# Kernel optimization log

Measured on AMD Instinct MI355X. Metric: run time of the kernel, lower is better.

## Reference

```python
import jax, jax.numpy as jnp
import numpy as np

N = 4_194_304  # total points
C = 2          # classes: 0=ground, 1=plant
B = 8          # number of point clouds in the batch
SIGMA_L = 0.1
SIGMA_R = 0.4
CLAMP_FACTOR = 2.0
MIN_VAL = 0.1
FOCAL_GAMMA = 2.0
FOCAL_ALPHA = 1.0
LOSS_WEIGHT = 1.0


def setup_inputs() -> dict:
    key = jax.random.key(0)
    k1, k2, k3 = jax.random.split(key, 3)
    pred = jax.random.normal(k1, (N, C), dtype=jnp.float32)
    coord = jax.random.normal(k2, (N, 3), dtype=jnp.float32)
    segment = jax.random.randint(k3, (N,), 0, C, dtype=jnp.int32)
    # pointcept-style cumulative offsets: equal-sized clouds, offset[-1] == N
    offset = (jnp.arange(1, B + 1, dtype=jnp.int32) * (N // B))
    return {"pred": pred, "coord": coord, "segment": segment, "offset": offset}


def _gauss_weights(z, segment, batch):
    # per-cloud z_ground_max (fallback: z.min) and z_plant_min (fallback: z.max)
    neg_inf = jnp.array(-jnp.inf, z.dtype)
    pos_inf = jnp.array(jnp.inf, z.dtype)
    gmax = jax.ops.segment_max(jnp.where(segment == 0, z, neg_inf), batch, num_segments=B)
    pmin = jax.ops.segment_min(jnp.where(segment == 1, z, pos_inf), batch, num_segments=B)
    has_g = jax.ops.segment_sum((segment == 0).astype(z.dtype), batch, num_segments=B) > 0
    has_p = jax.ops.segment_sum((segment == 1).astype(z.dtype), batch, num_segments=B) > 0
    zmin = jax.ops.segment_min(z, batch, num_segments=B)
    zmax = jax.ops.segment_max(z, batch, num_segments=B)
    g = jnp.where(has_g, gmax, zmin)
    p = jnp.where(has_p, pmin, zmax)
    mu_b = g + (p - g) * 0.5  # (B,)
    mu = mu_b[batch]          # (N,)
    d = z - mu
    w_left = jnp.exp(-(d * d) / (2.0 * SIGMA_L * SIGMA_L))
    w_right = jnp.exp(-(d * d) / (2.0 * SIGMA_R * SIGMA_R))
    w_right = jnp.where(d > CLAMP_FACTOR * SIGMA_R, jnp.array(MIN_VAL, z.dtype), w_right)
    return jnp.where(z <= mu, w_left, w_right)


def reference(pred, coord, segment, offset):
    n = pred.shape[0]
    # offset2batch: per-point batch id from cumulative offsets
    batch = jnp.searchsorted(offset, jnp.arange(n, dtype=offset.dtype), side='right')
    # cross entropy (reduction='none')
    logp = jax.nn.log_softmax(pred, axis=1)              # (N, C)
    logp_t = jnp.take_along_axis(logp, segment[:, None], axis=1)[:, 0]  # (N,)
    seg_loss = (-logp_t) * LOSS_WEIGHT
    # focal reweighting (computed under no_grad in the original)
    p_t = jax.lax.stop_gradient(jnp.exp(logp_t))
    focal_weight = FOCAL_ALPHA * (1.0 - p_t) ** FOCAL_GAMMA
    seg_loss = seg_loss * focal_weight
    # asymmetric gaussian z-weighting, segment-conditioned per cloud
    weights = _gauss_weights(coord[:, 2], segment, batch)
    return jnp.mean(seg_loss * weights)
```

## Files before the change

### kernel.cpp

```cpp
#include <hip/hip_runtime.h>
#include <math.h>

#define T   1024
#define NB  512

__device__ __forceinline__ unsigned enc_f(float f) {
    unsigned b = __float_as_uint(f);
    return (b & 0x80000000u) ? ~b : (b | 0x80000000u);
}
__device__ __forceinline__ float dec_f(unsigned u) {
    unsigned b = (u & 0x80000000u) ? (u ^ 0x80000000u) : ~u;
    return __uint_as_float(b);
}
#define ENC_NEG_INF 0x007FFFFFu
#define ENC_POS_INF 0xFF800000u
__device__ __forceinline__ unsigned ident_w(int w) {
    return (w < 8 || w >= 24) ? ENC_NEG_INF : ENC_POS_INF;
}

#define SLOT(base, blk) ((base) + 64 + (blk) * 32)
#define PART_W  20000u

#define CNT_B(ii, bdst) do { bdst = 0; \
    _Pragma("unroll") for (int j_ = 0; j_ < 8; ++j_) bdst += ((ii) >= roff[j_]); } while (0)

#define FLUSH_LDS(bb, g_, p_, mn_, mx_) do { \
    atomicMax(&s_stats[      (bb)], enc_f(g_));  \
    atomicMin(&s_stats[ 8  + (bb)], enc_f(p_));  \
    atomicMin(&s_stats[16  + (bb)], enc_f(mn_)); \
    atomicMax(&s_stats[24  + (bb)], enc_f(mx_)); } while (0)

#define STAT4(z0, z1, z2, z3, s) do { \
    lmn = fminf(lmn, fminf(fminf(z0, z1), fminf(z2, z3))); \
    lmx = fmaxf(lmx, fmaxf(fmaxf(z0, z1), fmaxf(z2, z3))); \
    lg = fmaxf(lg, ((s).x == 0) ? z0 : -INFINITY); \
    lg = fmaxf(lg, ((s).y == 0) ? z1 : -INFINITY); \
    lg = fmaxf(lg, ((s).z == 0) ? z2 : -INFINITY); \
    lg = fmaxf(lg, ((s).w == 0) ? z3 : -INFINITY); \
    lp = fminf(lp, ((s).x != 0) ? z0 : INFINITY); \
    lp = fminf(lp, ((s).y != 0) ? z1 : INFINITY); \
    lp = fminf(lp, ((s).z != 0) ? z2 : INFINITY); \
    lp = fminf(lp, ((s).w != 0) ? z3 : INFINITY); } while (0)

__device__ __forceinline__ float point_loss(float p0, float p1, int s, float z, float mu) {
    float margin = (s == 0) ? (p0 - p1) : (p1 - p0);
    float t   = __expf(-margin);
    float den = 1.0f + t;
    float inv = __builtin_amdgcn_rcpf(den);
    float om  = t * inv;
    float loss = __logf(den) * om * om;
    float d  = z - mu;
    float cf = (z <= mu) ? 50.0f : 3.125f;
    float w  = __expf(-d * d * cf);
    if (z > mu && d > 0.8f) w = 0.1f;
    return loss * w;
}

__global__ __launch_bounds__(T, 8) void k_stats(
        const float* __restrict__ coord, const int* __restrict__ segment,
        const int* __restrict__ offset, unsigned* __restrict__ ws, int n, int nb) {
    __shared__ unsigned s_stats[32];
    const int tid = threadIdx.x;
    if (tid < 32) s_stats[tid] = ident_w(tid);
    int roff[8];
    #pragma unroll
    for (int j = 0; j < 8; ++j) roff[j] = (j < nb) ? offset[j] : 0x7FFFFFFF;
    __syncthreads();

    int chunk = (n + (int)gridDim.x - 1) / (int)gridDim.x;
    chunk = (chunk + 3) & ~3;
    const int start = blockIdx.x * chunk;
    const int end   = min(n, start + chunk);

    if (start < end) {
        int ba = 0, bb = 0;
        #pragma unroll
        for (int j = 0; j < 8; ++j) { ba += (start >= roff[j]); bb += ((end - 1) >= roff[j]); }
        float lg = -INFINITY, lp = INFINITY, lmn = INFINITY, lmx = -INFINITY;

        if (ba == bb && (end - start) == 8 * T) {
            const float4* c4 = (const float4*)coord;
            const int4*   s4 = (const int4*)segment;
            const int q0 = (start >> 2) + tid, q1 = q0 + T;
            float4 a0 = c4[3 * q0 + 0], b0 = c4[3 * q0 + 1], c0 = c4[3 * q0 + 2];
            float4 a1 = c4[3 * q1 + 0], b1 = c4[3 * q1 + 1], c1 = c4[3 * q1 + 2];
            int4   s0 = s4[q0],        s1 = s4[q1];
            const float x0 = a0.z, x1 = b0.y, x2 = c0.x, x3 = c0.w;
            STAT4(x0, x1, x2, x3, s0);
            const float y0 = a1.z, y1 = b1.y, y2 = c1.x, y3 = c1.w;
            STAT4(y0, y1, y2, y3, s1);
            #pragma unroll
            for (int m = 32; m; m >>= 1) {
                lg  = fmaxf(lg,  __shfl_xor(lg,  m, 64));
                lp  = fminf(lp,  __shfl_xor(lp,  m, 64));
                lmn = fminf(lmn, __shfl_xor(lmn, m, 64));
                lmx = fmaxf(lmx, __shfl_xor(lmx, m, 64));
            }
            if ((tid & 63) == 0) FLUSH_LDS(ba, lg, lp, lmn, lmx);
        } else if (ba == bb && ((end - start) % (4 * T) == 0)) {
            const float4* c4 = (const float4*)coord;
            const int4*   s4 = (const int4*)segment;
            for (int p0 = start; p0 < end; p0 += 4 * T) {
                const int q = (p0 >> 2) + tid;
                float4 a = c4[3 * q + 0], b = c4[3 * q + 1], c = c4[3 * q + 2];
                int4   s = s4[q];
                const float x0 = a.z, x1 = b.y, x2 = c.x, x3 = c.w;
                STAT4(x0, x1, x2, x3, s);
            }
            #pragma unroll
            for (int m = 32; m; m >>= 1) {
                lg  = fmaxf(lg,  __shfl_xor(lg,  m, 64));
                lp  = fminf(lp,  __shfl_xor(lp,  m, 64));
                lmn = fminf(lmn, __shfl_xor(lmn, m, 64));
                lmx = fmaxf(lmx, __shfl_xor(lmx, m, 64));
            }
            if ((tid & 63) == 0) FLUSH_LDS(ba, lg, lp, lmn, lmx);
        } else {
            int curb = -1;
            for (int i = start + tid; i < end; i += T) {
                float z = coord[3 * i + 2]; int s = segment[i], b;
                CNT_B(i, b);
                if (b != curb) {
                    if (curb >= 0) FLUSH_LDS(curb, lg, lp, lmn, lmx);
                    lg = -INFINITY; lp = INFINITY; lmn = INFINITY; lmx = -INFINITY;
                    curb = b;
                }
                lmn = fminf(lmn, z); lmx = fmaxf(lmx, z);
                if (s == 0) lg = fmaxf(lg, z); else lp = fminf(lp, z);
            }
            if (curb >= 0) FLUSH_LDS(curb, lg, lp, lmn, lmx);
        }
    }
    __syncthreads();
    if (tid < 32) SLOT(ws, blockIdx.x)[tid] = s_stats[tid];
}

__global__ __launch_bounds__(T, 8) void k_loss(
        const float* __restrict__ pred, const float* __restrict__ coord,
        const int* __restrict__ segment, const int* __restrict__ offset,
        unsigned* __restrict__ ws, int n, int nb) {
    __shared__ unsigned s_comb[32];
    __shared__ float    s_mu[8];
    __shared__ float    s_part[T / 64];
    const int tid = threadIdx.x;
    int roff[8];
    #pragma unroll
    for (int j = 0; j < 8; ++j) roff[j] = (j < nb) ? offset[j] : 0x7FFFFFFF;

    if (tid < 32) s_comb[tid] = ident_w(tid);
    __syncthreads();
    {
        const int w = tid & 31, g = tid >> 5;
        unsigned v = ident_w(w);
        #pragma unroll
        for (int j = 0; j < NB / 32; ++j) {
            unsigned u = SLOT((const unsigned*)ws, g * (NB / 32) + j)[w];
            v = (w < 8 || w >= 24) ? max(v, u) : min(v, u);
        }
        if (w < 8 || w >= 24) atomicMax(&s_comb[w], v);
        else                  atomicMin(&s_comb[w], v);
    }
    __syncthreads();
    if (tid < 8) {
        unsigned ug = s_comb[tid], up = s_comb[8 + tid];
        float g = dec_f(ug), p = dec_f(up);
        if (ug == ENC_NEG_INF) g = dec_f(s_comb[16 + tid]);
        if (up == ENC_POS_INF) p = dec_f(s_comb[24 + tid]);
        s_mu[tid] = g + (p - g) * 0.5f;
    }
    __syncthreads();

    int chunk = (n + (int)gridDim.x - 1) / (int)gridDim.x;
    chunk = (chunk + 3) & ~3;
    const int start = blockIdx.x * chunk;
    const int end   = min(n, start + chunk);

    float lsum = 0.0f;
    if (start < end) {
        int ba = 0, bb = 0;
        #pragma unroll
        for (int j = 0; j < 8; ++j) { ba += (start >= roff[j]); bb += ((end - 1) >= roff[j]); }

        if (ba == bb && (end - start) == 8 * T) {
            const float mu = s_mu[ba];
            const float4* p4 = (const float4*)pred;
            const float4* c4 = (const float4*)coord;
            const int4*   s4 = (const int4*)segment;
            const int q0 = (start >> 2) + tid, q1 = q0 + T;
            float4 pa0 = p4[2 * q0 + 0], pb0 = p4[2 * q0 + 1];
            float4 pa1 = p4[2 * q1 + 0], pb1 = p4[2 * q1 + 1];
            float4 a0 = c4[3 * q0 + 0], b0 = c4[3 * q0 + 1], c0 = c4[3 * q0 + 2];
            float4 a1 = c4[3 * q1 + 0], b1 = c4[3 * q1 + 1], c1 = c4[3 * q1 + 2];
            int4   s0 = s4[q0],        s1 = s4[q1];
            lsum += point_loss(pa0.x, pa0.y, s0.x, a0.z, mu);
            lsum += point_loss(pa0.z, pa0.w, s0.y, b0.y, mu);
            lsum += point_loss(pb0.x, pb0.y, s0.z, c0.x, mu);
            lsum += point_loss(pb0.z, pb0.w, s0.w, c0.w, mu);
            lsum += point_loss(pa1.x, pa1.y, s1.x, a1.z, mu);
            lsum += point_loss(pa1.z, pa1.w, s1.y, b1.y, mu);
            lsum += point_loss(pb1.x, pb1.y, s1.z, c1.x, mu);
            lsum += point_loss(pb1.z, pb1.w, s1.w, c1.w, mu);
        } else if (ba == bb && ((end - start) % (4 * T) == 0)) {
            const float mu = s_mu[ba];
            const float4* p4 = (const float4*)pred;
            const float4* c4 = (const float4*)coord;
            const int4*   s4 = (const int4*)segment;
            for (int p0 = start; p0 < end; p0 += 4 * T) {
                const int q = (p0 >> 2) + tid;
                float4 pa = p4[2 * q + 0], pb = p4[2 * q + 1];
                float4 a  = c4[3 * q + 0], b = c4[3 * q + 1], c = c4[3 * q + 2];
                int4   s  = s4[q];
                lsum += point_loss(pa.x, pa.y, s.x, a.z, mu);
                lsum += point_loss(pa.z, pa.w, s.y, b.y, mu);
                lsum += point_loss(pb.x, pb.y, s.z, c.x, mu);
                lsum += point_loss(pb.z, pb.w, s.w, c.w, mu);
            }
        } else {
            const float2* pred2 = (const float2*)pred;
            for (int i = start + tid; i < end; i += T) {
                int b; CNT_B(i, b);
                float2 pp = pred2[i];
                lsum += point_loss(pp.x, pp.y, segment[i], coord[3 * i + 2], s_mu[b]);
            }
        }
    }

    #pragma unroll
    for (int off = 32; off > 0; off >>= 1) lsum += __shfl_down(lsum, off, 64);
    if ((tid & 63) == 0) s_part[tid >> 6] = lsum;
    __syncthreads();
    if (tid == 0) {
        float t = 0.0f;
        #pragma unroll
        for (int wv = 0; wv < T / 64; ++wv) t += s_part[wv];
        ((float*)(ws + PART_W))[blockIdx.x] = t;
    }
}

__global__ __launch_bounds__(NB) void k_final(
        const unsigned* __restrict__ ws, float* __restrict__ out, int n) {
    __shared__ float sp[NB];
    const int tid = threadIdx.x;
    sp[tid] = ((const float*)(ws + PART_W))[tid];
    __syncthreads();
    if (tid == 0) {
        double v = 0.0;
        for (int i = 0; i < NB; ++i) v += (double)sp[i];
        out[0] = (float)(v / (double)n);
    }
}

extern "C" void kernel_launch(void* const* d_in, const int* in_sizes, int n_in,
                              void* d_out, int out_size, void* d_ws, size_t ws_size,
                              hipStream_t stream) {
    const float* pred    = (const float*)d_in[0];
    const float* coord   = (const float*)d_in[1];
    const int*   segment = (const int*)d_in[2];
    const int*   offset  = (const int*)d_in[3];
    const int n  = in_sizes[2];
    const int nb = in_sizes[3];
    unsigned* ws = (unsigned*)d_ws;

    hipLaunchKernelGGL(k_stats, dim3(NB), dim3(T), 0, stream,
                       coord, segment, offset, ws, n, nb);
    hipLaunchKernelGGL(k_loss, dim3(NB), dim3(T), 0, stream,
                       pred, coord, segment, offset, ws, n, nb);
    hipLaunchKernelGGL(k_final, dim3(1), dim3(NB), 0, stream,
                       ws, (float*)d_out, n);
}
```

Before: 131.0 us.

## Use many small blocks and add hierarchical stats-combine kernel

Blocks shrink from 1024 to 256 threads, and the grid grows from 512 to 4096 blocks, each covering 4*T points. This is meant to spread work more evenly over the CUs and raise occupancy. A new k_mu kernel reduces the 4096 per-block stat records into 32 intermediate records, so each k_loss block reads only 32 records instead of every block's partials. The final reduction changes to sum 4096 partials. The cost is an extra kernel launch and a second reduction level.

```diff
diff --git a/kernel.cpp b/kernel.cpp
--- a/kernel.cpp
+++ b/kernel.cpp
@@ -1,8 +1,10 @@
 #include <hip/hip_runtime.h>
 #include <math.h>
 
-#define T   1024
-#define NB  512
+#define T    256
+#define NB   4096
+#define NM   32
+#define RPM  (NB / NM)
 
 __device__ __forceinline__ unsigned enc_f(float f) {
     unsigned b = __float_as_uint(f);
@@ -19,7 +21,8 @@
 }
 
 #define SLOT(base, blk) ((base) + 64 + (blk) * 32)
-#define PART_W  20000u
+#define SREC(base, m)   ((base) + 131200u + (m) * 32)
+#define PART_W  140000u
 
 #define CNT_B(ii, bdst) do { bdst = 0; \
     _Pragma("unroll") for (int j_ = 0; j_ < 8; ++j_) bdst += ((ii) >= roff[j_]); } while (0)
@@ -56,7 +59,7 @@
     return loss * w;
 }
 
-__global__ __launch_bounds__(T, 8) void k_stats(
+__global__ __launch_bounds__(T) void k_stats(
         const float* __restrict__ coord, const int* __restrict__ segment,
         const int* __restrict__ offset, unsigned* __restrict__ ws, int n, int nb) {
     __shared__ unsigned s_stats[32];
@@ -78,17 +81,13 @@
         for (int j = 0; j < 8; ++j) { ba += (start >= roff[j]); bb += ((end - 1) >= roff[j]); }
         float lg = -INFINITY, lp = INFINITY, lmn = INFINITY, lmx = -INFINITY;
 
-        if (ba == bb && (end - start) == 8 * T) {
-            const float4* c4 = (const float4*)coord;
-            const int4*   s4 = (const int4*)segment;
-            const int q0 = (start >> 2) + tid, q1 = q0 + T;
-            float4 a0 = c4[3 * q0 + 0], b0 = c4[3 * q0 + 1], c0 = c4[3 * q0 + 2];
-            float4 a1 = c4[3 * q1 + 0], b1 = c4[3 * q1 + 1], c1 = c4[3 * q1 + 2];
-            int4   s0 = s4[q0],        s1 = s4[q1];
-            const float x0 = a0.z, x1 = b0.y, x2 = c0.x, x3 = c0.w;
-            STAT4(x0, x1, x2, x3, s0);
-            const float y0 = a1.z, y1 = b1.y, y2 = c1.x, y3 = c1.w;
-            STAT4(y0, y1, y2, y3, s1);
+        if (ba == bb && (end - start) == 4 * T) {
+            const float4* c4 = (const float4*)coord;
+            const int4*   s4 = (const int4*)segment;
+            const int q = (start >> 2) + tid;
+            float4 a = c4[3 * q + 0], b = c4[3 * q + 1], c = c4[3 * q + 2];
+            int4   s = s4[q];
+            STAT4(a.z, b.y, c.x, c.w, s);
             #pragma unroll
             for (int m = 32; m; m >>= 1) {
                 lg  = fmaxf(lg,  __shfl_xor(lg,  m, 64));
@@ -104,8 +103,7 @@
                 const int q = (p0 >> 2) + tid;
                 float4 a = c4[3 * q + 0], b = c4[3 * q + 1], c = c4[3 * q + 2];
                 int4   s = s4[q];
-                const float x0 = a.z, x1 = b.y, x2 = c.x, x3 = c.w;
-                STAT4(x0, x1, x2, x3, s);
+                STAT4(a.z, b.y, c.x, c.w, s);
             }
             #pragma unroll
             for (int m = 32; m; m >>= 1) {
@@ -135,7 +133,25 @@
     if (tid < 32) SLOT(ws, blockIdx.x)[tid] = s_stats[tid];
 }
 
-__global__ __launch_bounds__(T, 8) void k_loss(
+__global__ __launch_bounds__(1024) void k_mu(unsigned* __restrict__ ws) {
+    __shared__ unsigned s_comb[32];
+    const int tid = threadIdx.x;
+    if (tid < 32) s_comb[tid] = ident_w(tid);
+    __syncthreads();
+    const int w = tid & 31, g = tid >> 5;
+    unsigned v = ident_w(w);
+    #pragma unroll
+    for (int k = 0; k < RPM / 32; ++k) {
+        unsigned u = SLOT((const unsigned*)ws, blockIdx.x * RPM + g + 32 * k)[w];
+        v = (w < 8 || w >= 24) ? max(v, u) : min(v, u);
+    }
+    if (w < 8 || w >= 24) atomicMax(&s_comb[w], v);
+    else                  atomicMin(&s_comb[w], v);
+    __syncthreads();
+    if (tid < 32) SREC(ws, blockIdx.x)[tid] = s_comb[tid];
+}
+
+__global__ __launch_bounds__(T) void k_loss(
         const float* __restrict__ pred, const float* __restrict__ coord,
         const int* __restrict__ segment, const int* __restrict__ offset,
         unsigned* __restrict__ ws, int n, int nb) {
@@ -153,8 +169,8 @@
         const int w = tid & 31, g = tid >> 5;
         unsigned v = ident_w(w);
         #pragma unroll
-        for (int j = 0; j < NB / 32; ++j) {
-            unsigned u = SLOT((const unsigned*)ws, g * (NB / 32) + j)[w];
+        for (int j = 0; j < NM / 8; ++j) {
+            unsigned u = SREC((const unsigned*)ws, g * (NM / 8) + j)[w];
             v = (w < 8 || w >= 24) ? max(v, u) : min(v, u);
         }
         if (w < 8 || w >= 24) atomicMax(&s_comb[w], v);
@@ -181,25 +197,19 @@
         #pragma unroll
         for (int j = 0; j < 8; ++j) { ba += (start >= roff[j]); bb += ((end - 1) >= roff[j]); }
 
-        if (ba == bb && (end - start) == 8 * T) {
+        if (ba == bb && (end - start) == 4 * T) {
             const float mu = s_mu[ba];
             const float4* p4 = (const float4*)pred;
             const float4* c4 = (const float4*)coord;
             const int4*   s4 = (const int4*)segment;
-            const int q0 = (start >> 2) + tid, q1 = q0 + T;
-            float4 pa0 = p4[2 * q0 + 0], pb0 = p4[2 * q0 + 1];
-            float4 pa1 = p4[2 * q1 + 0], pb1 = p4[2 * q1 + 1];
-            float4 a0 = c4[3 * q0 + 0], b0 = c4[3 * q0 + 1], c0 = c4[3 * q0 + 2];
-            float4 a1 = c4[3 * q1 + 0], b1 = c4[3 * q1 + 1], c1 = c4[3 * q1 + 2];
-            int4   s0 = s4[q0],        s1 = s4[q1];
-            lsum += point_loss(pa0.x, pa0.y, s0.x, a0.z, mu);
-            lsum += point_loss(pa0.z, pa0.w, s0.y, b0.y, mu);
-            lsum += point_loss(pb0.x, pb0.y, s0.z, c0.x, mu);
-            lsum += point_loss(pb0.z, pb0.w, s0.w, c0.w, mu);
-            lsum += point_loss(pa1.x, pa1.y, s1.x, a1.z, mu);
-            lsum += point_loss(pa1.z, pa1.w, s1.y, b1.y, mu);
-            lsum += point_loss(pb1.x, pb1.y, s1.z, c1.x, mu);
-            lsum += point_loss(pb1.z, pb1.w, s1.w, c1.w, mu);
+            const int q = (start >> 2) + tid;
+            float4 pa = p4[2 * q + 0], pb = p4[2 * q + 1];
+            float4 a  = c4[3 * q + 0], b = c4[3 * q + 1], c = c4[3 * q + 2];
+            int4   s  = s4[q];
+            lsum += point_loss(pa.x, pa.y, s.x, a.z, mu);
+            lsum += point_loss(pa.z, pa.w, s.y, b.y, mu);
+            lsum += point_loss(pb.x, pb.y, s.z, c.x, mu);
+            lsum += point_loss(pb.z, pb.w, s.w, c.w, mu);
         } else if (ba == bb && ((end - start) % (4 * T) == 0)) {
             const float mu = s_mu[ba];
             const float4* p4 = (const float4*)pred;
@@ -237,15 +247,19 @@
     }
 }
 
-__global__ __launch_bounds__(NB) void k_final(
+__global__ __launch_bounds__(1024) void k_final(
         const unsigned* __restrict__ ws, float* __restrict__ out, int n) {
-    __shared__ float sp[NB];
-    const int tid = threadIdx.x;
-    sp[tid] = ((const float*)(ws + PART_W))[tid];
+    __shared__ double sp[1024];
+    const int tid = threadIdx.x;
+    const float* part = (const float*)(ws + PART_W);
+    double d = 0.0;
+    #pragma unroll
+    for (int k = 0; k < NB / 1024; ++k) d += (double)part[tid * (NB / 1024) + k];
+    sp[tid] = d;
     __syncthreads();
     if (tid == 0) {
         double v = 0.0;
-        for (int i = 0; i < NB; ++i) v += (double)sp[i];
+        for (int i = 0; i < 1024; ++i) v += sp[i];
         out[0] = (float)(v / (double)n);
     }
 }
@@ -263,8 +277,9 @@
 
     hipLaunchKernelGGL(k_stats, dim3(NB), dim3(T), 0, stream,
                        coord, segment, offset, ws, n, nb);
+    hipLaunchKernelGGL(k_mu, dim3(NM), dim3(1024), 0, stream, ws);
     hipLaunchKernelGGL(k_loss, dim3(NB), dim3(T), 0, stream,
                        pred, coord, segment, offset, ws, n, nb);
-    hipLaunchKernelGGL(k_final, dim3(1), dim3(NB), 0, stream,
+    hipLaunchKernelGGL(k_final, dim3(1), dim3(1024), 0, stream,
                        ws, (float*)d_out, n);
 }
```

Result: slower. 135.1 us (+3.1%).
